# Performance work log

Measured on AMD Instinct MI355X. Metric: run time of the kernel, lower is better.

## Reference

```python
import jax, jax.numpy as jnp
import numpy as np

NUM_CODES = 8192
CODE_DIM = 256
BETA = 0.25


def setup_inputs() -> dict:
    key = jax.random.key(0)
    k1, k2 = jax.random.split(key)
    z_e = jax.random.normal(k1, (32, 1024, CODE_DIM), dtype=jnp.float32)
    # matches nn.init.uniform_(weight, -1/num_codes, 1/num_codes)
    codebook = jax.random.uniform(
        k2, (NUM_CODES, CODE_DIM), dtype=jnp.float32,
        minval=-1.0 / NUM_CODES, maxval=1.0 / NUM_CODES)
    return {"z_e": z_e, "codebook": codebook}


def reference(z_e, codebook):
    b, n, d = z_e.shape
    z_flat = z_e.reshape(-1, d)                       # [B*N, D]
    # squared L2 distance via ||z||^2 - 2 z.e + ||e||^2
    z_sq = jnp.sum(z_flat * z_flat, axis=1, keepdims=True)      # [B*N, 1]
    e_sq = jnp.sum(codebook * codebook, axis=1)[None, :]         # [1, K]
    ze = z_flat @ codebook.T                                     # [B*N, K]
    dist = z_sq - 2.0 * ze + e_sq
    codes_idx = jnp.argmin(dist, axis=1)                         # [B*N]
    z_q = codebook[codes_idx].reshape(b, n, d)
    # straight-through estimator
    z_q_st = z_e + jax.lax.stop_gradient(z_q - z_e)
    vq_loss = (jnp.mean((jax.lax.stop_gradient(z_q) - z_e) ** 2)
               + BETA * jnp.mean((z_q - jax.lax.stop_gradient(z_e)) ** 2))
    return z_q_st, vq_loss, codes_idx.reshape(b, n)
```

## Files before the change

kernel.cpp:

```cpp
#include <hip/hip_runtime.h>


#define NUM_CODES 8192
#define DIM 256
#define TOTAL_ROWS 32768
#define ROWS_PER_BLOCK 128
#define TILE_K 32
#define NCHUNK (NUM_CODES / TILE_K)
#define OUT_LOSS_OFF 8388608
#define OUT_IDX_OFF 8388609
#define LOSS_SCALE (1.25 / 8388608.0)
#define DOT_MARGIN 3.5e-4f
#define CLIST_MAX 160

typedef __attribute__((ext_vector_type(8))) short bf16x8;
typedef __attribute__((ext_vector_type(4))) float f32x4;

#define AS1 __attribute__((address_space(1)))
#define AS3 __attribute__((address_space(3)))
static __device__ __forceinline__ void gload_lds16(const void* g, void* l) {
    __builtin_amdgcn_global_load_lds((const AS1 unsigned int*)(uintptr_t)g,
                                     (AS3 unsigned int*)(uintptr_t)l, 16, 0, 0);
}

static __device__ __forceinline__ unsigned short f2bf(float f) {
    union { float f; unsigned u; } v; v.f = f;
    return (unsigned short)((v.u + 0x7FFF + ((v.u >> 16) & 1)) >> 16);
}

static __device__ __forceinline__ float sq32(float v) {
    float s = v * v;
    asm("" : "+v"(s));
    return s;
}

static __device__ __forceinline__ float pairwise256_sq(
        const float* __restrict__ base, int l) {
    const int h = (l >> 3) & 1, j = l & 7;
    const float* p = base + h * 128 + j;
    float acc = sq32(p[0]);
    #pragma unroll
    for (int m = 1; m < 16; ++m) acc += sq32(p[m * 8]);
    acc += __shfl_xor(acc, 1);
    acc += __shfl_xor(acc, 2);
    acc += __shfl_xor(acc, 4);
    acc += __shfl_xor(acc, 8);
    return acc;
}

__global__ __launch_bounds__(64) void rowsq_kernel(const float* __restrict__ x,
                                                   float* __restrict__ sq) {
    const int l = threadIdx.x;
    const long row = ((long)blockIdx.x << 2) + (l >> 4);
    float s = pairwise256_sq(x + row * DIM, l);
    if ((l & 15) == 0) sq[row] = s;
}

__global__ __launch_bounds__(256) void cvt_swz_kernel(
        const float* __restrict__ cb, uint4* __restrict__ pbz) {
    const int o = blockIdx.x * 256 + threadIdx.x;
    const int ch = o >> 10, idx = o & 1023;
    const int c = idx >> 5, sw = idx & 31;
    const int s = sw ^ (c & 7);
    const float* p = cb + ((long)(ch * TILE_K + c) << 8) + s * 8;
    float4 a = *(const float4*)p, b = *(const float4*)(p + 4);
    union { unsigned short us[8]; uint4 v; } r;
    r.us[0] = f2bf(a.x); r.us[1] = f2bf(a.y); r.us[2] = f2bf(a.z); r.us[3] = f2bf(a.w);
    r.us[4] = f2bf(b.x); r.us[5] = f2bf(b.y); r.us[6] = f2bf(b.z); r.us[7] = f2bf(b.w);
    pbz[o] = r.v;
}

__global__ __launch_bounds__(256, 1) void vq_scan_kernel(
        const float* __restrict__ z, const float* __restrict__ cb,
        const uint4* __restrict__ pbz,
        const float* __restrict__ esq, const float* __restrict__ zsq,
        float* __restrict__ out, double* __restrict__ loss_acc) {
    __shared__ bf16x8 ct[2][TILE_K * 32];
    __shared__ unsigned long long winner[ROWS_PER_BLOCK];
    __shared__ unsigned clist[4][CLIST_MAX];
    __shared__ int ccnt[4];

    const int tid = threadIdx.x;
    const int w = tid >> 6, l = tid & 63;
    const int cl = l & 15, g = l >> 4;
    const int x7 = cl & 7;
    const long rowbase = (long)blockIdx.x * ROWS_PER_BLOCK;
    const int wrowL = w * 32;

    if (tid < ROWS_PER_BLOCK) winner[tid] = ~0ull;
    if (tid < 4) ccnt[tid] = 0;

    bf16x8 af[2][8];
    #pragma unroll
    for (int t = 0; t < 2; ++t) {
        const long r = rowbase + wrowL + t * 16 + cl;
        #pragma unroll
        for (int ks = 0; ks < 8; ++ks) {
            const float* p = z + r * DIM + ks * 32 + g * 8;
            float4 a = *(const float4*)p, b = *(const float4*)(p + 4);
            bf16x8 v;
            v[0] = f2bf(a.x); v[1] = f2bf(a.y); v[2] = f2bf(a.z); v[3] = f2bf(a.w);
            v[4] = f2bf(b.x); v[5] = f2bf(b.y); v[6] = f2bf(b.z); v[7] = f2bf(b.w);
            af[t][ks] = v;
        }
    }

    #define STAGE(ch_, buf_) { \
        const char* gs_ = (const char*)pbz + ((long)(ch_) << 14) + (w << 10) + (l << 4); \
        char* ld_ = (char*)&ct[buf_][0] + (w << 10); \
        _Pragma("unroll") \
        for (int i_ = 0; i_ < 4; ++i_) \
            gload_lds16(gs_ + i_ * 4096, ld_ + i_ * 4096); \
    }

    STAGE(0, 0);
    __syncthreads();

    unsigned k1a[8], k2a[8], k3a[8];
    #pragma unroll
    for (int i = 0; i < 8; ++i) { k1a[i] = 0u; k2a[i] = 0u; k3a[i] = 0u; }

    #define INSERT(rs_, sv_, kc_) { \
        unsigned u_ = __float_as_uint(sv_); \
        u_ ^= ((unsigned)((int)u_ >> 31)) | 0x80000000u; \
        u_ = (u_ & 0xFFFFE000u) | (kc_); \
        unsigned mx_ = k1a[rs_] > u_ ? k1a[rs_] : u_; \
        unsigned mn_ = k1a[rs_] > u_ ? u_ : k1a[rs_]; \
        k1a[rs_] = mx_; \
        unsigned mx2_ = k2a[rs_] > mn_ ? k2a[rs_] : mn_; \
        unsigned mn2_ = k2a[rs_] > mn_ ? mn_ : k2a[rs_]; \
        k2a[rs_] = mx2_; \
        k3a[rs_] = k3a[rs_] > mn2_ ? k3a[rs_] : mn2_; \
    }

    for (int ch = 0; ch < NCHUNK; ++ch) {
        const int buf = ch & 1;
        if (ch + 1 < NCHUNK) STAGE(ch + 1, buf ^ 1);

        bf16x8 breg[16];
        #pragma unroll
        for (int ks = 0; ks < 8; ++ks)
            #pragma unroll
            for (int nt = 0; nt < 2; ++nt)
                breg[ks * 2 + nt] =
                    ct[buf][nt * 512 + cl * 32 + (((ks << 2) + g) ^ x7)];

        f32x4 acc[2][2];
        #pragma unroll
        for (int t = 0; t < 2; ++t)
            #pragma unroll
            for (int n = 0; n < 2; ++n) acc[t][n] = (f32x4){0.f, 0.f, 0.f, 0.f};
        #pragma unroll
        for (int ks = 0; ks < 8; ++ks) {
            #pragma unroll
            for (int nt = 0; nt < 2; ++nt) {
                acc[0][nt] = __builtin_amdgcn_mfma_f32_16x16x32_bf16(
                    af[0][ks], breg[ks * 2 + nt], acc[0][nt], 0, 0, 0);
                acc[1][nt] = __builtin_amdgcn_mfma_f32_16x16x32_bf16(
                    af[1][ks], breg[ks * 2 + nt], acc[1][nt], 0, 0, 0);
            }
        }

        const unsigned kc0 = (unsigned)(ch * TILE_K + cl);
        #pragma unroll
        for (int t = 0; t < 2; ++t)
            #pragma unroll
            for (int nt = 0; nt < 2; ++nt)
                #pragma unroll
                for (int r = 0; r < 4; ++r)
                    INSERT(t * 4 + r, acc[t][nt][r], nt ? (kc0 + 16) : kc0);

        __syncthreads();
    }

    #define COLLECT(rs_, T_, R_) { \
        unsigned gm_ = k1a[rs_]; \
        unsigned t_; \
        t_ = __shfl_xor(gm_, 1); gm_ = gm_ > t_ ? gm_ : t_; \
        t_ = __shfl_xor(gm_, 2); gm_ = gm_ > t_ ? gm_ : t_; \
        t_ = __shfl_xor(gm_, 4); gm_ = gm_ > t_ ? gm_ : t_; \
        t_ = __shfl_xor(gm_, 8); gm_ = gm_ > t_ ? gm_ : t_; \
        float gs_ = __uint_as_float((gm_ & 0x80000000u) ? (gm_ ^ 0x80000000u) : ~gm_); \
        unsigned tu_ = __float_as_uint(gs_ - DOT_MARGIN); \
        tu_ ^= ((unsigned)((int)tu_ >> 31)) | 0x80000000u; \
        const unsigned thr_ = tu_ & 0xFFFFE000u; \
        const unsigned rowp_ = (unsigned)(wrowL + T_ * 16 + g * 4 + R_) << 16; \
        if (k1a[rs_] >= thr_) { int p_ = atomicAdd(&ccnt[w], 1); \
            if (p_ < CLIST_MAX) clist[w][p_] = rowp_ | (k1a[rs_] & 0x1FFFu); } \
        if (k2a[rs_] >= thr_) { int p_ = atomicAdd(&ccnt[w], 1); \
            if (p_ < CLIST_MAX) clist[w][p_] = rowp_ | (k2a[rs_] & 0x1FFFu); } \
        if (k3a[rs_] >= thr_) { int p_ = atomicAdd(&ccnt[w], 1); \
            if (p_ < CLIST_MAX) clist[w][p_] = rowp_ | (k3a[rs_] & 0x1FFFu); } \
    }
    COLLECT(0, 0, 0); COLLECT(1, 0, 1); COLLECT(2, 0, 2); COLLECT(3, 0, 3);
    COLLECT(4, 1, 0); COLLECT(5, 1, 1); COLLECT(6, 1, 2); COLLECT(7, 1, 3);
    __syncthreads();

    const int n = ccnt[w] < CLIST_MAX ? ccnt[w] : CLIST_MAX;
    for (int j = 0; j < n; ++j) {
        const unsigned e = clist[w][j];
        const int rowL = e >> 16;
        const int code = e & 0x1FFF;
        const long grow = rowbase + rowL;
        float4 zz = *(const float4*)(z + grow * DIM + l * 4);
        float4 cc = *(const float4*)(cb + (long)code * DIM + l * 4);
        double dd = (double)zz.x * cc.x + (double)zz.y * cc.y
                  + (double)zz.z * cc.z + (double)zz.w * cc.w;
        dd += __shfl_xor(dd, 1);
        dd += __shfl_xor(dd, 2);
        dd += __shfl_xor(dd, 4);
        dd += __shfl_xor(dd, 8);
        dd += __shfl_xor(dd, 16);
        dd += __shfl_xor(dd, 32);
        const float s = (zsq[grow] - 2.0f * (float)dd) + esq[code];
        if (l == 0) {
            const unsigned long long p =
                ((unsigned long long)__float_as_uint(s) << 32) | (unsigned)code;
            if (p < winner[rowL]) winner[rowL] = p;
        }
    }

    double lacc = 0.0;
    #pragma unroll 1
    for (int i = 0; i < 32; ++i) {
        const int rowL = wrowL + i;
        const long grow = rowbase + rowL;
        const int kw = (int)(winner[rowL] & 0x1FFFull);
        float4 zz = *(const float4*)(z + grow * DIM + l * 4);
        float4 cq = *(const float4*)(cb + (long)kw * DIM + l * 4);
        float4 oo;
        oo.x = zz.x + (cq.x - zz.x); oo.y = zz.y + (cq.y - zz.y);
        oo.z = zz.z + (cq.z - zz.z); oo.w = zz.w + (cq.w - zz.w);
        *(float4*)(out + grow * DIM + l * 4) = oo;
        if (l == 0) out[OUT_IDX_OFF + grow] = (float)kw;
        const double d0 = (double)cq.x - zz.x, d1 = (double)cq.y - zz.y;
        const double d2 = (double)cq.z - zz.z, d3 = (double)cq.w - zz.w;
        lacc += d0 * d0 + d1 * d1 + d2 * d2 + d3 * d3;
    }
    lacc += __shfl_xor(lacc, 1);
    lacc += __shfl_xor(lacc, 2);
    lacc += __shfl_xor(lacc, 4);
    lacc += __shfl_xor(lacc, 8);
    lacc += __shfl_xor(lacc, 16);
    lacc += __shfl_xor(lacc, 32);
    if (l == 0) atomicAdd(loss_acc, lacc);
}

__global__ void vq_finalize_kernel(const double* __restrict__ loss_acc,
                                   float* __restrict__ out) {
    out[OUT_LOSS_OFF] = (float)(*loss_acc * LOSS_SCALE);
}

extern "C" void kernel_launch(void* const* d_in, const int* in_sizes, int n_in,
                              void* d_out, int out_size, void* d_ws, size_t ws_size,
                              hipStream_t stream) {
    const float* z  = (const float*)d_in[0];
    const float* cb = (const float*)d_in[1];
    float* out = (float*)d_out;
    double* loss_acc = (double*)d_ws;
    float* esq = (float*)((char*)d_ws + 4096);
    float* zsq = (float*)((char*)d_ws + 40960);
    uint4* pbz = (uint4*)((char*)d_ws + 262144);

    hipMemsetAsync(d_ws, 0, 8, stream);
    rowsq_kernel<<<NUM_CODES / 4, 64, 0, stream>>>(cb, esq);
    rowsq_kernel<<<TOTAL_ROWS / 4, 64, 0, stream>>>(z, zsq);
    cvt_swz_kernel<<<NUM_CODES * TILE_K / 256, 256, 0, stream>>>(cb, pbz);
    vq_scan_kernel<<<TOTAL_ROWS / ROWS_PER_BLOCK, 256, 0, stream>>>(
        z, cb, pbz, esq, zsq, out, loss_acc);
    vq_finalize_kernel<<<1, 1, 0, stream>>>(loss_acc, out);
}
```

Before: 347.2 us.

## Halve rows per block for two blocks per CU and fuse z norm computation

```diff
diff --git a/kernel.cpp b/kernel.cpp
--- a/kernel.cpp
+++ b/kernel.cpp
@@ -4,14 +4,14 @@
 #define NUM_CODES 8192
 #define DIM 256
 #define TOTAL_ROWS 32768
-#define ROWS_PER_BLOCK 128
+#define ROWS_PER_BLOCK 64
 #define TILE_K 32
 #define NCHUNK (NUM_CODES / TILE_K)
 #define OUT_LOSS_OFF 8388608
 #define OUT_IDX_OFF 8388609
 #define LOSS_SCALE (1.25 / 8388608.0)
 #define DOT_MARGIN 3.5e-4f
-#define CLIST_MAX 160
+#define CLIST_MAX 128
 
 typedef __attribute__((ext_vector_type(8))) short bf16x8;
 typedef __attribute__((ext_vector_type(4))) float f32x4;
@@ -70,13 +70,13 @@
     pbz[o] = r.v;
 }
 
-__global__ __launch_bounds__(256, 1) void vq_scan_kernel(
+__global__ __launch_bounds__(256, 2) void vq_scan_kernel(
         const float* __restrict__ z, const float* __restrict__ cb,
-        const uint4* __restrict__ pbz,
-        const float* __restrict__ esq, const float* __restrict__ zsq,
+        const uint4* __restrict__ pbz, const float* __restrict__ esq,
         float* __restrict__ out, double* __restrict__ loss_acc) {
     __shared__ bf16x8 ct[2][TILE_K * 32];
     __shared__ unsigned long long winner[ROWS_PER_BLOCK];
+    __shared__ float zsql[ROWS_PER_BLOCK];
     __shared__ unsigned clist[4][CLIST_MAX];
     __shared__ int ccnt[4];
 
@@ -85,15 +85,24 @@
     const int cl = l & 15, g = l >> 4;
     const int x7 = cl & 7;
     const long rowbase = (long)blockIdx.x * ROWS_PER_BLOCK;
-    const int wrowL = w * 32;
+    const int wrowL = w * 16;
 
     if (tid < ROWS_PER_BLOCK) winner[tid] = ~0ull;
     if (tid < 4) ccnt[tid] = 0;
 
-    bf16x8 af[2][8];
-    #pragma unroll
-    for (int t = 0; t < 2; ++t) {
-        const long r = rowbase + wrowL + t * 16 + cl;
+    #define STAGE(ch_, buf_) { \
+        const char* gs_ = (const char*)pbz + ((long)(ch_) << 14) + (w << 10) + (l << 4); \
+        char* ld_ = (char*)&ct[buf_][0] + (w << 10); \
+        _Pragma("unroll") \
+        for (int i_ = 0; i_ < 4; ++i_) \
+            gload_lds16(gs_ + i_ * 4096, ld_ + i_ * 4096); \
+    }
+
+    STAGE(0, 0);
+
+    bf16x8 af[8];
+    {
+        const long r = rowbase + wrowL + cl;
         #pragma unroll
         for (int ks = 0; ks < 8; ++ks) {
             const float* p = z + r * DIM + ks * 32 + g * 8;
@@ -101,24 +110,20 @@
             bf16x8 v;
             v[0] = f2bf(a.x); v[1] = f2bf(a.y); v[2] = f2bf(a.z); v[3] = f2bf(a.w);
             v[4] = f2bf(b.x); v[5] = f2bf(b.y); v[6] = f2bf(b.z); v[7] = f2bf(b.w);
-            af[t][ks] = v;
+            af[ks] = v;
         }
     }
-
-    #define STAGE(ch_, buf_) { \
-        const char* gs_ = (const char*)pbz + ((long)(ch_) << 14) + (w << 10) + (l << 4); \
-        char* ld_ = (char*)&ct[buf_][0] + (w << 10); \
-        _Pragma("unroll") \
-        for (int i_ = 0; i_ < 4; ++i_) \
-            gload_lds16(gs_ + i_ * 4096, ld_ + i_ * 4096); \
-    }
-
-    STAGE(0, 0);
+    #pragma unroll
+    for (int p4 = 0; p4 < 4; ++p4) {
+        const int r0 = wrowL + p4 * 4 + (l >> 4);
+        float s = pairwise256_sq(z + (rowbase + r0) * DIM, l);
+        if ((l & 15) == 0) zsql[r0] = s;
+    }
     __syncthreads();
 
-    unsigned k1a[8], k2a[8], k3a[8];
+    unsigned k1a[4], k2a[4], k3a[4];
     #pragma unroll
-    for (int i = 0; i < 8; ++i) { k1a[i] = 0u; k2a[i] = 0u; k3a[i] = 0u; }
+    for (int i = 0; i < 4; ++i) { k1a[i] = 0u; k2a[i] = 0u; k3a[i] = 0u; }
 
     #define INSERT(rs_, sv_, kc_) { \
         unsigned u_ = __float_as_uint(sv_); \
@@ -145,35 +150,28 @@
                 breg[ks * 2 + nt] =
                     ct[buf][nt * 512 + cl * 32 + (((ks << 2) + g) ^ x7)];
 
-        f32x4 acc[2][2];
-        #pragma unroll
-        for (int t = 0; t < 2; ++t)
+        f32x4 acc[2];
+        acc[0] = (f32x4){0.f, 0.f, 0.f, 0.f};
+        acc[1] = (f32x4){0.f, 0.f, 0.f, 0.f};
+        #pragma unroll
+        for (int ks = 0; ks < 8; ++ks) {
+            acc[0] = __builtin_amdgcn_mfma_f32_16x16x32_bf16(
+                af[ks], breg[ks * 2 + 0], acc[0], 0, 0, 0);
+            acc[1] = __builtin_amdgcn_mfma_f32_16x16x32_bf16(
+                af[ks], breg[ks * 2 + 1], acc[1], 0, 0, 0);
+        }
+
+        const unsigned kc0 = (unsigned)(ch * TILE_K + cl);
+        #pragma unroll
+        for (int nt = 0; nt < 2; ++nt)
             #pragma unroll
-            for (int n = 0; n < 2; ++n) acc[t][n] = (f32x4){0.f, 0.f, 0.f, 0.f};
-        #pragma unroll
-        for (int ks = 0; ks < 8; ++ks) {
-            #pragma unroll
-            for (int nt = 0; nt < 2; ++nt) {
-                acc[0][nt] = __builtin_amdgcn_mfma_f32_16x16x32_bf16(
-                    af[0][ks], breg[ks * 2 + nt], acc[0][nt], 0, 0, 0);
-                acc[1][nt] = __builtin_amdgcn_mfma_f32_16x16x32_bf16(
-                    af[1][ks], breg[ks * 2 + nt], acc[1][nt], 0, 0, 0);
-            }
-        }
-
-        const unsigned kc0 = (unsigned)(ch * TILE_K + cl);
-        #pragma unroll
-        for (int t = 0; t < 2; ++t)
-            #pragma unroll
-            for (int nt = 0; nt < 2; ++nt)
-                #pragma unroll
-                for (int r = 0; r < 4; ++r)
-                    INSERT(t * 4 + r, acc[t][nt][r], nt ? (kc0 + 16) : kc0);
+            for (int r = 0; r < 4; ++r)
+                INSERT(r, acc[nt][r], nt ? (kc0 + 16) : kc0);
 
         __syncthreads();
     }
 
-    #define COLLECT(rs_, T_, R_) { \
+    #define COLLECT(rs_, R_) { \
         unsigned gm_ = k1a[rs_]; \
         unsigned t_; \
         t_ = __shfl_xor(gm_, 1); gm_ = gm_ > t_ ? gm_ : t_; \
@@ -184,7 +182,7 @@
         unsigned tu_ = __float_as_uint(gs_ - DOT_MARGIN); \
         tu_ ^= ((unsigned)((int)tu_ >> 31)) | 0x80000000u; \
         const unsigned thr_ = tu_ & 0xFFFFE000u; \
-        const unsigned rowp_ = (unsigned)(wrowL + T_ * 16 + g * 4 + R_) << 16; \
+        const unsigned rowp_ = (unsigned)(wrowL + g * 4 + R_) << 16; \
         if (k1a[rs_] >= thr_) { int p_ = atomicAdd(&ccnt[w], 1); \
             if (p_ < CLIST_MAX) clist[w][p_] = rowp_ | (k1a[rs_] & 0x1FFFu); } \
         if (k2a[rs_] >= thr_) { int p_ = atomicAdd(&ccnt[w], 1); \
@@ -192,8 +190,7 @@
         if (k3a[rs_] >= thr_) { int p_ = atomicAdd(&ccnt[w], 1); \
             if (p_ < CLIST_MAX) clist[w][p_] = rowp_ | (k3a[rs_] & 0x1FFFu); } \
     }
-    COLLECT(0, 0, 0); COLLECT(1, 0, 1); COLLECT(2, 0, 2); COLLECT(3, 0, 3);
-    COLLECT(4, 1, 0); COLLECT(5, 1, 1); COLLECT(6, 1, 2); COLLECT(7, 1, 3);
+    COLLECT(0, 0); COLLECT(1, 1); COLLECT(2, 2); COLLECT(3, 3);
     __syncthreads();
 
     const int n = ccnt[w] < CLIST_MAX ? ccnt[w] : CLIST_MAX;
@@ -212,7 +209,7 @@
         dd += __shfl_xor(dd, 8);
         dd += __shfl_xor(dd, 16);
         dd += __shfl_xor(dd, 32);
-        const float s = (zsq[grow] - 2.0f * (float)dd) + esq[code];
+        const float s = (zsql[rowL] - 2.0f * (float)dd) + esq[code];
         if (l == 0) {
             const unsigned long long p =
                 ((unsigned long long)__float_as_uint(s) << 32) | (unsigned)code;
@@ -222,7 +219,7 @@
 
     double lacc = 0.0;
     #pragma unroll 1
-    for (int i = 0; i < 32; ++i) {
+    for (int i = 0; i < 16; ++i) {
         const int rowL = wrowL + i;
         const long grow = rowbase + rowL;
         const int kw = (int)(winner[rowL] & 0x1FFFull);
@@ -259,14 +256,12 @@
     float* out = (float*)d_out;
     double* loss_acc = (double*)d_ws;
     float* esq = (float*)((char*)d_ws + 4096);
-    float* zsq = (float*)((char*)d_ws + 40960);
     uint4* pbz = (uint4*)((char*)d_ws + 262144);
 
     hipMemsetAsync(d_ws, 0, 8, stream);
     rowsq_kernel<<<NUM_CODES / 4, 64, 0, stream>>>(cb, esq);
-    rowsq_kernel<<<TOTAL_ROWS / 4, 64, 0, stream>>>(z, zsq);
     cvt_swz_kernel<<<NUM_CODES * TILE_K / 256, 256, 0, stream>>>(cb, pbz);
     vq_scan_kernel<<<TOTAL_ROWS / ROWS_PER_BLOCK, 256, 0, stream>>>(
-        z, cb, pbz, esq, zsq, out, loss_acc);
+        z, cb, pbz, esq, out, loss_acc);
     vq_finalize_kernel<<<1, 1, 0, stream>>>(loss_acc, out);
 }
```

New measurement: 285.0 us. -17.9%, faster.

## Halve block rows to 64 with two blocks per CU and fuse z-norm computation

Applied to the files above, without the earlier changes.

```diff
diff --git a/kernel.cpp b/kernel.cpp
--- a/kernel.cpp
+++ b/kernel.cpp
@@ -4,7 +4,7 @@
 #define NUM_CODES 8192
 #define DIM 256
 #define TOTAL_ROWS 32768
-#define ROWS_PER_BLOCK 128
+#define ROWS_PER_BLOCK 64
 #define TILE_K 32
 #define NCHUNK (NUM_CODES / TILE_K)
 #define OUT_LOSS_OFF 8388608
@@ -70,15 +70,15 @@
     pbz[o] = r.v;
 }
 
-__global__ __launch_bounds__(256, 1) void vq_scan_kernel(
+__global__ __launch_bounds__(128, 2) void vq_scan_kernel(
         const float* __restrict__ z, const float* __restrict__ cb,
-        const uint4* __restrict__ pbz,
-        const float* __restrict__ esq, const float* __restrict__ zsq,
+        const uint4* __restrict__ pbz, const float* __restrict__ esq,
         float* __restrict__ out, double* __restrict__ loss_acc) {
     __shared__ bf16x8 ct[2][TILE_K * 32];
     __shared__ unsigned long long winner[ROWS_PER_BLOCK];
-    __shared__ unsigned clist[4][CLIST_MAX];
-    __shared__ int ccnt[4];
+    __shared__ float zsql[ROWS_PER_BLOCK];
+    __shared__ unsigned clist[2][CLIST_MAX];
+    __shared__ int ccnt[2];
 
     const int tid = threadIdx.x;
     const int w = tid >> 6, l = tid & 63;
@@ -87,8 +87,18 @@
     const long rowbase = (long)blockIdx.x * ROWS_PER_BLOCK;
     const int wrowL = w * 32;
 
-    if (tid < ROWS_PER_BLOCK) winner[tid] = ~0ull;
-    if (tid < 4) ccnt[tid] = 0;
+    if (l < 32) winner[wrowL + l] = ~0ull;
+    if (l == 0) ccnt[w] = 0;
+
+    #define STAGE(ch_, buf_) { \
+        const char* gs_ = (const char*)pbz + ((long)(ch_) << 14) + (w << 10) + (l << 4); \
+        char* ld_ = (char*)&ct[buf_][0] + (w << 10); \
+        _Pragma("unroll") \
+        for (int i_ = 0; i_ < 8; ++i_) \
+            gload_lds16(gs_ + i_ * 2048, ld_ + i_ * 2048); \
+    }
+
+    STAGE(0, 0);
 
     bf16x8 af[2][8];
     #pragma unroll
@@ -104,16 +114,12 @@
             af[t][ks] = v;
         }
     }
-
-    #define STAGE(ch_, buf_) { \
-        const char* gs_ = (const char*)pbz + ((long)(ch_) << 14) + (w << 10) + (l << 4); \
-        char* ld_ = (char*)&ct[buf_][0] + (w << 10); \
-        _Pragma("unroll") \
-        for (int i_ = 0; i_ < 4; ++i_) \
-            gload_lds16(gs_ + i_ * 4096, ld_ + i_ * 4096); \
-    }
-
-    STAGE(0, 0);
+    #pragma unroll
+    for (int p4 = 0; p4 < 8; ++p4) {
+        const int r0 = wrowL + p4 * 4 + (l >> 4);
+        float s = pairwise256_sq(z + (rowbase + r0) * DIM, l);
+        if ((l & 15) == 0) zsql[r0] = s;
+    }
     __syncthreads();
 
     unsigned k1a[8], k2a[8], k3a[8];
@@ -180,16 +186,17 @@
         t_ = __shfl_xor(gm_, 2); gm_ = gm_ > t_ ? gm_ : t_; \
         t_ = __shfl_xor(gm_, 4); gm_ = gm_ > t_ ? gm_ : t_; \
         t_ = __shfl_xor(gm_, 8); gm_ = gm_ > t_ ? gm_ : t_; \
-        float gs_ = __uint_as_float((gm_ & 0x80000000u) ? (gm_ ^ 0x80000000u) : ~gm_); \
-        unsigned tu_ = __float_as_uint(gs_ - DOT_MARGIN); \
+        unsigned sb_ = (gm_ & 0x80000000u) ? (gm_ ^ 0x80000000u) : ~gm_; \
+        float gs_ = __uint_as_float(sb_) - DOT_MARGIN; \
+        unsigned tu_ = __float_as_uint(gs_); \
         tu_ ^= ((unsigned)((int)tu_ >> 31)) | 0x80000000u; \
-        const unsigned thr_ = tu_ & 0xFFFFE000u; \
+        tu_ &= 0xFFFFE000u; \
         const unsigned rowp_ = (unsigned)(wrowL + T_ * 16 + g * 4 + R_) << 16; \
-        if (k1a[rs_] >= thr_) { int p_ = atomicAdd(&ccnt[w], 1); \
+        if (k1a[rs_] >= tu_) { int p_ = atomicAdd(&ccnt[w], 1); \
             if (p_ < CLIST_MAX) clist[w][p_] = rowp_ | (k1a[rs_] & 0x1FFFu); } \
-        if (k2a[rs_] >= thr_) { int p_ = atomicAdd(&ccnt[w], 1); \
+        if (k2a[rs_] >= tu_) { int p_ = atomicAdd(&ccnt[w], 1); \
             if (p_ < CLIST_MAX) clist[w][p_] = rowp_ | (k2a[rs_] & 0x1FFFu); } \
-        if (k3a[rs_] >= thr_) { int p_ = atomicAdd(&ccnt[w], 1); \
+        if (k3a[rs_] >= tu_) { int p_ = atomicAdd(&ccnt[w], 1); \
             if (p_ < CLIST_MAX) clist[w][p_] = rowp_ | (k3a[rs_] & 0x1FFFu); } \
     }
     COLLECT(0, 0, 0); COLLECT(1, 0, 1); COLLECT(2, 0, 2); COLLECT(3, 0, 3);
@@ -212,13 +219,14 @@
         dd += __shfl_xor(dd, 8);
         dd += __shfl_xor(dd, 16);
         dd += __shfl_xor(dd, 32);
-        const float s = (zsq[grow] - 2.0f * (float)dd) + esq[code];
+        const float s = (zsql[rowL] - 2.0f * (float)dd) + esq[code];
         if (l == 0) {
             const unsigned long long p =
                 ((unsigned long long)__float_as_uint(s) << 32) | (unsigned)code;
             if (p < winner[rowL]) winner[rowL] = p;
         }
     }
+    __syncthreads();
 
     double lacc = 0.0;
     #pragma unroll 1
@@ -259,14 +267,12 @@
     float* out = (float*)d_out;
     double* loss_acc = (double*)d_ws;
     float* esq = (float*)((char*)d_ws + 4096);
-    float* zsq = (float*)((char*)d_ws + 40960);
     uint4* pbz = (uint4*)((char*)d_ws + 262144);
 
     hipMemsetAsync(d_ws, 0, 8, stream);
     rowsq_kernel<<<NUM_CODES / 4, 64, 0, stream>>>(cb, esq);
-    rowsq_kernel<<<TOTAL_ROWS / 4, 64, 0, stream>>>(z, zsq);
     cvt_swz_kernel<<<NUM_CODES * TILE_K / 256, 256, 0, stream>>>(cb, pbz);
-    vq_scan_kernel<<<TOTAL_ROWS / ROWS_PER_BLOCK, 256, 0, stream>>>(
-        z, cb, pbz, esq, zsq, out, loss_acc);
+    vq_scan_kernel<<<TOTAL_ROWS / ROWS_PER_BLOCK, 128, 0, stream>>>(
+        z, cb, pbz, esq, out, loss_acc);
     vq_finalize_kernel<<<1, 1, 0, stream>>>(loss_acc, out);
 }
```

New measurement: 411.2 us. +18.4%, slower.
